# Kernel optimization log

Measured on AMD Instinct MI355X. Metric: run time of the kernel, lower is better.

## Reference

```python
import jax, jax.numpy as jnp
import numpy as np

N = 131072
N_DIM = 128
NUM_LAYERS = 8
N_MID = NUM_LAYERS - 2  # middle (n_dim -> n_dim) layers


def _sigmoid_layer(h, u_un, w_un, log_a, b):
    # h: [N, in]; u_un: [out, in]; w_un: [out, out]; log_a, b: [out, 1]
    a = jnp.exp(log_a)                      # [out, 1]
    u = jax.nn.softmax(u_un, axis=1)        # row-softmax, matches Softmax(dim=1)
    w = jax.nn.softmax(w_un, axis=1)
    inner = h @ (a * u).T + b[:, 0]         # [N, out]
    return jax.nn.sigmoid(inner) @ w.T      # [N, out]


def setup_inputs() -> dict:
    key = jax.random.key(0)
    ks = jax.random.split(key, 24)
    d = N_DIM
    inp = {
        "x": jax.random.normal(ks[0], (N,), jnp.float32),
        "fy0": jax.random.normal(ks[1], (N,), jnp.float32),
        # first layer (in=2, out=d)
        "u0": jax.random.normal(ks[2], (d, 2), jnp.float32),
        "w0": jax.random.normal(ks[3], (d, d), jnp.float32),
        "la0": jax.random.normal(ks[4], (d, 1), jnp.float32),
        "b0": jax.random.normal(ks[5], (d, 1), jnp.float32),
        # middle layers stacked (in=d, out=d)
        "uM": jax.random.normal(ks[6], (N_MID, d, d), jnp.float32),
        "wM": jax.random.normal(ks[7], (N_MID, d, d), jnp.float32),
        "laM": jax.random.normal(ks[8], (N_MID, d, 1), jnp.float32),
        "bM": jax.random.normal(ks[9], (N_MID, d, 1), jnp.float32),
        # last layer (in=d, out=1)
        "uL": jax.random.normal(ks[10], (1, d), jnp.float32),
        "wL": jax.random.normal(ks[11], (1, 1), jnp.float32),
        "laL": jax.random.normal(ks[12], (1, 1), jnp.float32),
        "bL": jax.random.normal(ks[13], (1, 1), jnp.float32),
        # MLP 1 -> 50 -> 50 -> 1
        "W1": jax.random.normal(ks[14], (50, 1), jnp.float32) * 0.2,
        "b1": jax.random.normal(ks[15], (50,), jnp.float32) * 0.2,
        "W2": jax.random.normal(ks[16], (50, 50), jnp.float32) * 0.1,
        "b2": jax.random.normal(ks[17], (50,), jnp.float32) * 0.1,
        "W3": jax.random.normal(ks[18], (1, 50), jnp.float32) * 0.1,
        "b3": jax.random.normal(ks[19], (1,), jnp.float32) * 0.1,
    }
    return inp


def reference(x, fy0, u0, w0, la0, b0, uM, wM, laM, bM, uL, wL, laL, bL,
              W1, b1, W2, b2, W3, b3):
    # MLP feature net on fy0: [N,1] -> [N,1]
    h = jax.nn.relu(fy0[:, None] @ W1.T + b1)
    h = jax.nn.relu(h @ W2.T + b2)
    theta = h @ W3.T + b3                          # [N, 1]
    mono = jnp.concatenate([x[:, None], theta], 1)  # [N, 2]

    mono = _sigmoid_layer(mono, u0, w0, la0, b0)    # [N, d]

    def step(carry, p):
        u_un, w_un, log_a, b = p
        return _sigmoid_layer(carry, u_un, w_un, log_a, b), None

    mono, _ = jax.lax.scan(step, mono, (uM, wM, laM, bM))
    out = _sigmoid_layer(mono, uL, wL, laL, bL)     # [N, 1]
    return out[:, :, None]                          # [N, 1, 1] matches torch
```

## Files before the change

### kernel.cpp

```cpp
#include <hip/hip_runtime.h>
#include <cstdint>

typedef __attribute__((ext_vector_type(8))) _Float16 half8;
typedef __attribute__((ext_vector_type(4))) _Float16 half4;
typedef __attribute__((ext_vector_type(2))) _Float16 half2v;
typedef __attribute__((ext_vector_type(16))) float f32x16;
typedef __attribute__((ext_vector_type(4))) float f4;

#define LOG2E 1.44269504088896340f
#define KNL  (-1.44269504088896340f)

__device__ __forceinline__ float fast_exp(float x) { return __builtin_amdgcn_exp2f(LOG2E * x); }
__device__ __forceinline__ float sigmoidf(float v) {
    return __builtin_amdgcn_rcpf(1.f + __builtin_amdgcn_exp2f(KNL * v));
}
__device__ __forceinline__ float sig2(float y) {
    return __builtin_amdgcn_rcpf(1.f + __builtin_amdgcn_exp2f(y));
}
__device__ __forceinline__ unsigned pkz(float a, float b) {
    return __builtin_bit_cast(unsigned, __builtin_amdgcn_cvt_pkrtz(a, b));
}
__device__ __forceinline__ void swapl(unsigned& a, unsigned& b) {
    asm volatile("v_permlane32_swap_b32 %0, %1" : "+v"(a), "+v"(b));
}
__device__ __forceinline__ void swaplf(float& a, float& b) {
    asm volatile("v_permlane32_swap_b32 %0, %1" : "+v"(a), "+v"(b));
}
union BU { unsigned u[4]; half8 h; };

constexpr int A0X = 0, A0T = 128, B0O = 256, BMO = 384, VLO = 1152,
              W1P = 1280, B1P = 1344, B2P = 1408, W3P = 1472, CN = 1536;

constexpr int GOFF  = 0;
constexpr int W2HIO = 6 * 65536;
constexpr int W2LOO = W2HIO + 8192;
constexpr int CGOFF = W2LOO + 8192;

__global__ __launch_bounds__(256)
void prep_kernel(const float* __restrict__ u0, const float* __restrict__ w0,
                 const float* __restrict__ la0, const float* __restrict__ b0,
                 const float* __restrict__ uM, const float* __restrict__ wM,
                 const float* __restrict__ laM, const float* __restrict__ bM,
                 const float* __restrict__ uL, const float* __restrict__ laL,
                 const float* __restrict__ W1, const float* __restrict__ b1,
                 const float* __restrict__ W2, const float* __restrict__ b2,
                 const float* __restrict__ W3,
                 char* __restrict__ G, _Float16* __restrict__ W2hi,
                 _Float16* __restrict__ W2lo, float* __restrict__ CgF)
{
    __shared__ float Wl[128 * 136];
    __shared__ float Al[8 * 132];
    __shared__ float uls[128];

    const int tid = threadIdx.x, b = blockIdx.x;
    const bool mblk = (b < 96);
    const int l = mblk ? (b >> 4) : 6;

    {
        const float* Wsrc = (l == 0) ? w0 : wM + (l - 1) * 16384;
        const int r = tid >> 1, h = tid & 1;
        const float* rp = Wsrc + r * 128 + h * 64;
        f4 buf[16];
#pragma unroll
        for (int v = 0; v < 16; ++v) buf[v] = *(const f4*)(rp + 4 * v);
        float mx = -1e30f;
#pragma unroll
        for (int v = 0; v < 16; ++v)
#pragma unroll
            for (int e = 0; e < 4; ++e) mx = fmaxf(mx, buf[v][e]);
        mx = fmaxf(mx, __shfl_xor(mx, 1));
        float s = 0.f;
#pragma unroll
        for (int v = 0; v < 16; ++v)
#pragma unroll
            for (int e = 0; e < 4; ++e) { buf[v][e] = fast_exp(buf[v][e] - mx); s += buf[v][e]; }
        s += __shfl_xor(s, 1);
        float inv = 1.f / s;
#pragma unroll
        for (int v = 0; v < 16; ++v)
            *(f4*)(&Wl[r * 136 + h * 64 + 4 * v]) = buf[v] * inv;
    }

    if (mblk) {
        const int q = b & 15;
        const int rl = tid >> 5, part = tid & 31;
        const int gi = q * 8 + rl;
        {
            f4 ub = *(const f4*)(uM + (l * 128 + gi) * 128 + part * 4);
            float mx = fmaxf(fmaxf(ub[0], ub[1]), fmaxf(ub[2], ub[3]));
#pragma unroll
            for (int o = 1; o < 32; o <<= 1) mx = fmaxf(mx, __shfl_xor(mx, o));
            float s = 0.f;
#pragma unroll
            for (int e = 0; e < 4; ++e) { ub[e] = fast_exp(ub[e] - mx); s += ub[e]; }
#pragma unroll
            for (int o = 1; o < 32; o <<= 1) s += __shfl_xor(s, o);
            float sc = fast_exp(laM[l * 128 + gi]) / s;
            *(f4*)(&Al[rl * 132 + part * 4]) = ub * sc;
        }
        __syncthreads();
        const int j0 = (tid & 31) * 4;
        f4 acc = {};
        for (int k = 0; k < 128; ++k) {
            float a = Al[rl * 132 + k];
            acc += a * *(const f4*)(&Wl[k * 136 + j0]);
        }
        const int sw = (gi & 7) << 4;
        char* bh = G + l * 65536 + gi * 256;
        char* bl = bh + 32768;
        half4 hv, lv;
#pragma unroll
        for (int e = 0; e < 4; ++e) {
            float m = KNL * acc[e];
            _Float16 hh = (_Float16)m;
            hv[e] = hh;
            lv[e] = (_Float16)(m - (float)hh);
        }
        *(half4*)(bh + ((2 * j0) ^ sw)) = hv;
        *(half4*)(bl + ((2 * j0) ^ sw)) = lv;
    } else {
        if (tid < 64) {
            float v0 = uL[tid], v1 = uL[tid + 64];
            float mx = fmaxf(v0, v1);
#pragma unroll
            for (int o = 32; o; o >>= 1) mx = fmaxf(mx, __shfl_xor(mx, o));
            float e0 = fast_exp(v0 - mx), e1 = fast_exp(v1 - mx);
            float ssum = e0 + e1;
#pragma unroll
            for (int o = 32; o; o >>= 1) ssum += __shfl_xor(ssum, o);
            float aL = fast_exp(laL[0]) / ssum;
            uls[tid]      = e0 * aL;
            uls[tid + 64] = e1 * aL;
        }
        __syncthreads();
        if (tid < 128) {
            float s = 0.f;
            for (int k = 0; k < 128; ++k) s += uls[k] * Wl[k * 136 + tid];
            CgF[VLO + tid] = s;
        }
        if (tid < 128) {
            const int j = tid;
            float q0 = u0[2 * j], q1 = u0[2 * j + 1];
            float mx = fmaxf(q0, q1);
            float e0 = fast_exp(q0 - mx), e1 = fast_exp(q1 - mx);
            float a = fast_exp(la0[j]) / (e0 + e1);
            CgF[A0X + j] = KNL * a * e0;
            CgF[A0T + j] = KNL * a * e1;
            CgF[B0O + j] = KNL * b0[j];
        } else if (tid < 192) {
            const int t = tid - 128;
            CgF[W1P + t] = (t < 50) ? W1[t] : 0.f;
            CgF[B1P + t] = (t < 50) ? b1[t] : 0.f;
            CgF[B2P + t] = (t < 50) ? b2[t] : 0.f;
            CgF[W3P + t] = (t < 50) ? W3[t] : 0.f;
        }
        for (int i = tid; i < 768; i += 256) CgF[BMO + i] = KNL * bM[i];
        for (int i = tid; i < 4096; i += 256) {
            int r = i >> 6, c = i & 63;
            float v = (r < 50 && c < 50) ? W2[r * 50 + c] : 0.f;
            _Float16 h = (_Float16)v;
            W2hi[i] = h;
            W2lo[i] = (_Float16)(v - (float)h);
        }
    }
}


__device__ __forceinline__ void stage64(char* ls, const char* gs, int tid) {
#pragma unroll
    for (int i = 0; i < 16; ++i)
        __builtin_amdgcn_global_load_lds(
            (const __attribute__((address_space(1))) unsigned*)(uintptr_t)(gs + tid * 16 + i * 4096),
            (__attribute__((address_space(3))) unsigned*)(uintptr_t)(ls + tid * 16 + i * 4096),
            16, 0, 0);
}

__device__ __forceinline__ void epi_nt(const f32x16& a0, const f32x16& a1,
                                       half8& o00, half8& o01, half8& o10, half8& o11)
{
#pragma unroll
    for (int bt = 0; bt < 2; ++bt) {
        const f32x16& A = bt ? a1 : a0;
        unsigned p00 = pkz(sig2(A[0]),  sig2(A[1]));
        unsigned p01 = pkz(sig2(A[2]),  sig2(A[3]));
        unsigned p10 = pkz(sig2(A[4]),  sig2(A[5]));
        unsigned p11 = pkz(sig2(A[6]),  sig2(A[7]));
        unsigned p20 = pkz(sig2(A[8]),  sig2(A[9]));
        unsigned p21 = pkz(sig2(A[10]), sig2(A[11]));
        unsigned p30 = pkz(sig2(A[12]), sig2(A[13]));
        unsigned p31 = pkz(sig2(A[14]), sig2(A[15]));
        swapl(p00, p10); swapl(p01, p11);
        swapl(p20, p30); swapl(p21, p31);
        BU u0; u0.u[0] = p00; u0.u[1] = p01; u0.u[2] = p10; u0.u[3] = p11;
        BU u1; u1.u[0] = p20; u1.u[1] = p21; u1.u[2] = p30; u1.u[3] = p31;
        if (bt == 0) { o00 = u0.h; o01 = u1.h; }
        else         { o10 = u0.h; o11 = u1.h; }
    }
}

__device__ __forceinline__ void do_layer(const char* buf,
                                         const half8 (&Bin)[2][8], half8 (&Bout)[2][8],
                                         const float* __restrict__ biasK,
                                         int l31, int hi)
{
    const int sw = (l31 & 7) << 4;
#pragma unroll
    for (int nt = 0; nt < 4; ++nt) {
        f4 bv0 = *(const f4*)(biasK + 32 * nt + 4 * hi);
        f4 bv1 = *(const f4*)(biasK + 32 * nt + 8 + 4 * hi);
        f4 bv2 = *(const f4*)(biasK + 32 * nt + 16 + 4 * hi);
        f4 bv3 = *(const f4*)(biasK + 32 * nt + 24 + 4 * hi);
        f32x16 a0e = { bv0[0], bv0[1], bv0[2], bv0[3],
                       bv1[0], bv1[1], bv1[2], bv1[3],
                       bv2[0], bv2[1], bv2[2], bv2[3],
                       bv3[0], bv3[1], bv3[2], bv3[3] };
        f32x16 a1e = a0e;
        f32x16 a0o = {}, a1o = {};
        const char* rhi = buf + (nt * 32 + l31) * 256;
        const char* rlo = rhi + 32768;
        __builtin_amdgcn_s_setprio(1);
#pragma unroll
        for (int ks = 0; ks < 8; ks += 2) {
            const int offE = (ks * 32 + hi * 16) ^ sw;
            const int offO = ((ks + 1) * 32 + hi * 16) ^ sw;
            half8 AhE = *(const half8*)(rhi + offE);
            half8 AhO = *(const half8*)(rhi + offO);
            half8 AlE = *(const half8*)(rlo + offE);
            half8 AlO = *(const half8*)(rlo + offO);
            a0e = __builtin_amdgcn_mfma_f32_32x32x16_f16(AhE, Bin[0][ks],     a0e, 0, 0, 0);
            a1e = __builtin_amdgcn_mfma_f32_32x32x16_f16(AhE, Bin[1][ks],     a1e, 0, 0, 0);
            a0o = __builtin_amdgcn_mfma_f32_32x32x16_f16(AhO, Bin[0][ks + 1], a0o, 0, 0, 0);
            a1o = __builtin_amdgcn_mfma_f32_32x32x16_f16(AhO, Bin[1][ks + 1], a1o, 0, 0, 0);
            a0e = __builtin_amdgcn_mfma_f32_32x32x16_f16(AlE, Bin[0][ks],     a0e, 0, 0, 0);
            a1e = __builtin_amdgcn_mfma_f32_32x32x16_f16(AlE, Bin[1][ks],     a1e, 0, 0, 0);
            a0o = __builtin_amdgcn_mfma_f32_32x32x16_f16(AlO, Bin[0][ks + 1], a0o, 0, 0, 0);
            a1o = __builtin_amdgcn_mfma_f32_32x32x16_f16(AlO, Bin[1][ks + 1], a1o, 0, 0, 0);
        }
        __builtin_amdgcn_s_setprio(0);
        f32x16 a0 = a0e + a0o, a1 = a1e + a1o;
        epi_nt(a0, a1, Bout[0][2 * nt], Bout[0][2 * nt + 1],
               Bout[1][2 * nt], Bout[1][2 * nt + 1]);
    }
}

__global__ __launch_bounds__(256, 2)
void mono_main(const float* __restrict__ x, const float* __restrict__ fy0,
               const char* __restrict__ G,
               const _Float16* __restrict__ W2hi, const _Float16* __restrict__ W2lo,
               const float* __restrict__ CgF, const float* __restrict__ b3g,
               const float* __restrict__ bLg, float* __restrict__ out)
{
    extern __shared__ __align__(16) char sm[];

    const int tid = threadIdx.x;
    const int lane = tid & 63, wave = tid >> 6;
    const int l31 = lane & 31, hi = lane >> 5;
    const int row0 = blockIdx.x * 256 + wave * 64;

    stage64(sm, G, tid);
    const float b3s = b3g[0], bLs = bLg[0];

    float fy[2] = { fy0[row0 + l31], fy0[row0 + 32 + l31] };
    half8 Bm[2][4];
#pragma unroll
    for (int ks = 0; ks < 4; ++ks) {
        f4 w1a = *(const f4*)(CgF + W1P + 16 * ks + 8 * hi);
        f4 w1b = *(const f4*)(CgF + W1P + 16 * ks + 8 * hi + 4);
        f4 b1a = *(const f4*)(CgF + B1P + 16 * ks + 8 * hi);
        f4 b1b = *(const f4*)(CgF + B1P + 16 * ks + 8 * hi + 4);
#pragma unroll
        for (int bt = 0; bt < 2; ++bt) {
            BU u;
            u.u[0] = pkz(fmaxf(fy[bt] * w1a[0] + b1a[0], 0.f), fmaxf(fy[bt] * w1a[1] + b1a[1], 0.f));
            u.u[1] = pkz(fmaxf(fy[bt] * w1a[2] + b1a[2], 0.f), fmaxf(fy[bt] * w1a[3] + b1a[3], 0.f));
            u.u[2] = pkz(fmaxf(fy[bt] * w1b[0] + b1b[0], 0.f), fmaxf(fy[bt] * w1b[1] + b1b[1], 0.f));
            u.u[3] = pkz(fmaxf(fy[bt] * w1b[2] + b1b[2], 0.f), fmaxf(fy[bt] * w1b[3] + b1b[3], 0.f));
            Bm[bt][ks] = u.h;
        }
    }

    f32x16 a00 = {}, a01 = {}, a10 = {}, a11 = {};
#pragma unroll
    for (int nt = 0; nt < 2; ++nt)
#pragma unroll
        for (int ks = 0; ks < 4; ++ks) {
            half8 Ah = *(const half8*)(W2hi + (nt * 32 + l31) * 64 + ks * 16 + hi * 8);
            half8 Al = *(const half8*)(W2lo + (nt * 32 + l31) * 64 + ks * 16 + hi * 8);
            if (nt == 0) {
                a00 = __builtin_amdgcn_mfma_f32_32x32x16_f16(Ah, Bm[0][ks], a00, 0, 0, 0);
                a10 = __builtin_amdgcn_mfma_f32_32x32x16_f16(Ah, Bm[1][ks], a10, 0, 0, 0);
                a00 = __builtin_amdgcn_mfma_f32_32x32x16_f16(Al, Bm[0][ks], a00, 0, 0, 0);
                a10 = __builtin_amdgcn_mfma_f32_32x32x16_f16(Al, Bm[1][ks], a10, 0, 0, 0);
            } else {
                a01 = __builtin_amdgcn_mfma_f32_32x32x16_f16(Ah, Bm[0][ks], a01, 0, 0, 0);
                a11 = __builtin_amdgcn_mfma_f32_32x32x16_f16(Ah, Bm[1][ks], a11, 0, 0, 0);
                a01 = __builtin_amdgcn_mfma_f32_32x32x16_f16(Al, Bm[0][ks], a01, 0, 0, 0);
                a11 = __builtin_amdgcn_mfma_f32_32x32x16_f16(Al, Bm[1][ks], a11, 0, 0, 0);
            }
        }

    float tp0 = 0.f, tp1 = 0.f;
#pragma unroll
    for (int nt = 0; nt < 2; ++nt)
#pragma unroll
        for (int g = 0; g < 4; ++g) {
            f4 w3 = *(const f4*)(CgF + W3P + 32 * nt + 8 * g + 4 * hi);
            f4 b2v = *(const f4*)(CgF + B2P + 32 * nt + 8 * g + 4 * hi);
            const f32x16& A0 = nt ? a01 : a00;
            const f32x16& A1 = nt ? a11 : a10;
#pragma unroll
            for (int e = 0; e < 4; ++e) {
                tp0 += w3[e] * fmaxf(A0[4 * g + e] + b2v[e], 0.f);
                tp1 += w3[e] * fmaxf(A1[4 * g + e] + b2v[e], 0.f);
            }
        }
    swaplf(tp0, tp1);
    float th = tp0 + tp1 + b3s;
    float t0 = th, t1 = th;
    swaplf(t0, t1);

    float xr[2] = { x[row0 + l31], x[row0 + 32 + l31] };
    float thv[2] = { t0, t1 };
    half8 Bq[2][8], Bp[2][8];
#pragma unroll
    for (int ks = 0; ks < 8; ++ks) {
        f4 axa = *(const f4*)(CgF + A0X + 16 * ks + 8 * hi);
        f4 axb = *(const f4*)(CgF + A0X + 16 * ks + 8 * hi + 4);
        f4 ata = *(const f4*)(CgF + A0T + 16 * ks + 8 * hi);
        f4 atb = *(const f4*)(CgF + A0T + 16 * ks + 8 * hi + 4);
        f4 b0a = *(const f4*)(CgF + B0O + 16 * ks + 8 * hi);
        f4 b0b = *(const f4*)(CgF + B0O + 16 * ks + 8 * hi + 4);
#pragma unroll
        for (int bt = 0; bt < 2; ++bt) {
            BU u;
            u.u[0] = pkz(sig2(axa[0] * xr[bt] + ata[0] * thv[bt] + b0a[0]),
                         sig2(axa[1] * xr[bt] + ata[1] * thv[bt] + b0a[1]));
            u.u[1] = pkz(sig2(axa[2] * xr[bt] + ata[2] * thv[bt] + b0a[2]),
                         sig2(axa[3] * xr[bt] + ata[3] * thv[bt] + b0a[3]));
            u.u[2] = pkz(sig2(axb[0] * xr[bt] + atb[0] * thv[bt] + b0b[0]),
                         sig2(axb[1] * xr[bt] + atb[1] * thv[bt] + b0b[1]));
            u.u[3] = pkz(sig2(axb[2] * xr[bt] + atb[2] * thv[bt] + b0b[2]),
                         sig2(axb[3] * xr[bt] + atb[3] * thv[bt] + b0b[3]));
            Bq[bt][ks] = u.h;
        }
    }
    __syncthreads();

    do_layer(sm, Bq, Bp, CgF + BMO + 0 * 128, l31, hi);
    __syncthreads();
    stage64(sm, G + 1 * 65536, tid);
    __syncthreads();
    do_layer(sm, Bp, Bq, CgF + BMO + 1 * 128, l31, hi);
    __syncthreads();
    stage64(sm, G + 2 * 65536, tid);
    __syncthreads();
    do_layer(sm, Bq, Bp, CgF + BMO + 2 * 128, l31, hi);
    __syncthreads();
    stage64(sm, G + 3 * 65536, tid);
    __syncthreads();
    do_layer(sm, Bp, Bq, CgF + BMO + 3 * 128, l31, hi);
    __syncthreads();
    stage64(sm, G + 4 * 65536, tid);
    __syncthreads();
    do_layer(sm, Bq, Bp, CgF + BMO + 4 * 128, l31, hi);
    __syncthreads();
    stage64(sm, G + 5 * 65536, tid);
    __syncthreads();
    do_layer(sm, Bp, Bq, CgF + BMO + 5 * 128, l31, hi);

    float d0 = 0.f, d1 = 0.f;
#pragma unroll
    for (int ks = 0; ks < 8; ++ks) {
        f4 va = *(const f4*)(CgF + VLO + 16 * ks + 8 * hi);
        f4 vb = *(const f4*)(CgF + VLO + 16 * ks + 8 * hi + 4);
        half8 s0 = Bq[0][ks], s1 = Bq[1][ks];
#pragma unroll
        for (int e = 0; e < 4; ++e) {
            d0 += va[e] * (float)s0[e] + vb[e] * (float)s0[e + 4];
            d1 += va[e] * (float)s1[e] + vb[e] * (float)s1[e + 4];
        }
    }
    swaplf(d0, d1);
    out[row0 + lane] = sigmoidf(d0 + d1 + bLs);
}

extern "C" void kernel_launch(void* const* d_in, const int* in_sizes, int n_in,
                              void* d_out, int out_size, void* d_ws, size_t ws_size,
                              hipStream_t stream)
{
    const float* x   = (const float*)d_in[0];
    const float* fy0 = (const float*)d_in[1];
    const float* u0  = (const float*)d_in[2];
    const float* w0  = (const float*)d_in[3];
    const float* la0 = (const float*)d_in[4];
    const float* b0  = (const float*)d_in[5];
    const float* uM  = (const float*)d_in[6];
    const float* wM  = (const float*)d_in[7];
    const float* laM = (const float*)d_in[8];
    const float* bM  = (const float*)d_in[9];
    const float* uL  = (const float*)d_in[10];
    const float* laL = (const float*)d_in[12];
    const float* bL  = (const float*)d_in[13];
    const float* W1  = (const float*)d_in[14];
    const float* b1  = (const float*)d_in[15];
    const float* W2  = (const float*)d_in[16];
    const float* b2  = (const float*)d_in[17];
    const float* W3  = (const float*)d_in[18];
    const float* b3  = (const float*)d_in[19];
    float* out = (float*)d_out;

    char* ws = (char*)d_ws;
    char*     Gz   = ws + GOFF;
    _Float16* W2hi = (_Float16*)(ws + W2HIO);
    _Float16* W2lo = (_Float16*)(ws + W2LOO);
    float*    CgF  = (float*)(ws + CGOFF);

    prep_kernel<<<97, 256, 0, stream>>>(u0, w0, la0, b0, uM, wM, laM, bM,
                                        uL, laL, W1, b1, W2, b2, W3,
                                        Gz, W2hi, W2lo, CgF);

    static bool attr_set = false;
    if (!attr_set) {
        hipFuncSetAttribute((const void*)mono_main,
                            hipFuncAttributeMaxDynamicSharedMemorySize, 65536);
        attr_set = true;
    }
    mono_main<<<512, 256, 65536, stream>>>(x, fy0, Gz, W2hi, W2lo,
                                           CgF, b3, bL, out);
}
```

Baseline: 160.3 us.

## Double-buffer layer weights in LDS with 512-thread blocks

Doubles block size to 512 threads (256 blocks) and uses two 64KB LDS buffers, so the next layer's weights are loaded into one buffer while the current layer computes from the other. This removes the serialized stage-then-compute pattern. It also halves how often each CU copies weights from global memory, since eight waves now share one staged copy. In exchange it needs 128KB of LDS per block, and the larger launch bound may cut the per-thread register budget and cause spills.

```diff
diff --git a/kernel.cpp b/kernel.cpp
--- a/kernel.cpp
+++ b/kernel.cpp
@@ -3,7 +3,6 @@
 
 typedef __attribute__((ext_vector_type(8))) _Float16 half8;
 typedef __attribute__((ext_vector_type(4))) _Float16 half4;
-typedef __attribute__((ext_vector_type(2))) _Float16 half2v;
 typedef __attribute__((ext_vector_type(16))) float f32x16;
 typedef __attribute__((ext_vector_type(4))) float f4;
 
@@ -168,10 +167,10 @@
 
 __device__ __forceinline__ void stage64(char* ls, const char* gs, int tid) {
 #pragma unroll
-    for (int i = 0; i < 16; ++i)
+    for (int i = 0; i < 8; ++i)
         __builtin_amdgcn_global_load_lds(
-            (const __attribute__((address_space(1))) unsigned*)(uintptr_t)(gs + tid * 16 + i * 4096),
-            (__attribute__((address_space(3))) unsigned*)(uintptr_t)(ls + tid * 16 + i * 4096),
+            (const __attribute__((address_space(1))) unsigned*)(uintptr_t)(gs + tid * 16 + i * 8192),
+            (__attribute__((address_space(3))) unsigned*)(uintptr_t)(ls + tid * 16 + i * 8192),
             16, 0, 0);
 }
 
@@ -243,7 +242,7 @@
     }
 }
 
-__global__ __launch_bounds__(256, 2)
+__global__ __launch_bounds__(512, 2)
 void mono_main(const float* __restrict__ x, const float* __restrict__ fy0,
                const char* __restrict__ G,
                const _Float16* __restrict__ W2hi, const _Float16* __restrict__ W2lo,
@@ -251,13 +250,15 @@
                const float* __restrict__ bLg, float* __restrict__ out)
 {
     extern __shared__ __align__(16) char sm[];
+    char* buf0 = sm;
+    char* buf1 = sm + 65536;
 
     const int tid = threadIdx.x;
     const int lane = tid & 63, wave = tid >> 6;
     const int l31 = lane & 31, hi = lane >> 5;
-    const int row0 = blockIdx.x * 256 + wave * 64;
-
-    stage64(sm, G, tid);
+    const int row0 = blockIdx.x * 512 + wave * 64;
+
+    stage64(buf0, G, tid);
     const float b3s = b3g[0], bLs = bLg[0];
 
     float fy[2] = { fy0[row0 + l31], fy0[row0 + 32 + l31] };
@@ -346,27 +347,22 @@
     }
     __syncthreads();
 
-    do_layer(sm, Bq, Bp, CgF + BMO + 0 * 128, l31, hi);
-    __syncthreads();
-    stage64(sm, G + 1 * 65536, tid);
-    __syncthreads();
-    do_layer(sm, Bp, Bq, CgF + BMO + 1 * 128, l31, hi);
-    __syncthreads();
-    stage64(sm, G + 2 * 65536, tid);
-    __syncthreads();
-    do_layer(sm, Bq, Bp, CgF + BMO + 2 * 128, l31, hi);
-    __syncthreads();
-    stage64(sm, G + 3 * 65536, tid);
-    __syncthreads();
-    do_layer(sm, Bp, Bq, CgF + BMO + 3 * 128, l31, hi);
-    __syncthreads();
-    stage64(sm, G + 4 * 65536, tid);
-    __syncthreads();
-    do_layer(sm, Bq, Bp, CgF + BMO + 4 * 128, l31, hi);
-    __syncthreads();
-    stage64(sm, G + 5 * 65536, tid);
-    __syncthreads();
-    do_layer(sm, Bp, Bq, CgF + BMO + 5 * 128, l31, hi);
+    stage64(buf1, G + 1 * 65536, tid);
+    do_layer(buf0, Bq, Bp, CgF + BMO + 0 * 128, l31, hi);
+    __syncthreads();
+    stage64(buf0, G + 2 * 65536, tid);
+    do_layer(buf1, Bp, Bq, CgF + BMO + 1 * 128, l31, hi);
+    __syncthreads();
+    stage64(buf1, G + 3 * 65536, tid);
+    do_layer(buf0, Bq, Bp, CgF + BMO + 2 * 128, l31, hi);
+    __syncthreads();
+    stage64(buf0, G + 4 * 65536, tid);
+    do_layer(buf1, Bp, Bq, CgF + BMO + 3 * 128, l31, hi);
+    __syncthreads();
+    stage64(buf1, G + 5 * 65536, tid);
+    do_layer(buf0, Bq, Bp, CgF + BMO + 4 * 128, l31, hi);
+    __syncthreads();
+    do_layer(buf1, Bp, Bq, CgF + BMO + 5 * 128, l31, hi);
 
     float d0 = 0.f, d1 = 0.f;
 #pragma unroll
@@ -422,9 +418,9 @@
     static bool attr_set = false;
     if (!attr_set) {
         hipFuncSetAttribute((const void*)mono_main,
-                            hipFuncAttributeMaxDynamicSharedMemorySize, 65536);
+                            hipFuncAttributeMaxDynamicSharedMemorySize, 131072);
         attr_set = true;
     }
-    mono_main<<<512, 256, 65536, stream>>>(x, fy0, Gz, W2hi, W2lo,
-                                           CgF, b3, bL, out);
-}
+    mono_main<<<256, 512, 131072, stream>>>(x, fy0, Gz, W2hi, W2lo,
+                                            CgF, b3, bL, out);
+}
```

New measurement: 155.1 us. 1.03x faster.
